# Kernel tuning notes

Measured on AMD Instinct MI355X. Metric: run time of the kernel, lower is better.

The kernel has to match this reference:

```python
import jax, jax.numpy as jnp
import numpy as np

B, N, H, MEM, V = 512, 50, 256, 8, 40001
SCALE = 1.0 / float(np.sqrt(H))
NEG = -1e12


def sinusoid_table(n_pos, d):
    pos = np.arange(n_pos)[:, None].astype(np.float64)
    j = np.arange(d)[None, :]
    ang = pos / np.power(10000.0, 2 * (j // 2) / d)
    tab = np.zeros((n_pos, d))
    tab[:, 0::2] = np.sin(ang[:, 0::2])
    tab[:, 1::2] = np.cos(ang[:, 1::2])
    return jnp.asarray(tab, jnp.float32)

TAB = sinusoid_table(N, H)


def setup_inputs():
    key = jax.random.key(0)
    ks = jax.random.split(key, 40)
    s = 0.05
    rn = lambda k, shp, sc=s: jax.random.normal(k, shp, jnp.float32) * sc
    lengths = jax.random.randint(ks[0], (B,), 1, N + 1)
    mask = (jnp.arange(N)[None, :] < lengths[:, None]).astype(jnp.int32)
    item_flag = jax.random.randint(ks[1], (B, V - 1), 0, 2).astype(jnp.int32)
    inp = {
        'seq_emb_1': rn(ks[2], (B, N, H), 1.0),
        'seq_emb_2': rn(ks[3], (B, N, H), 1.0),
        'mask': mask,
        'item_flag': item_flag,
        # 2-layer GRU (torch layout: W_ih [3H,H], W_hh [3H,H])
        'gru_wih0': rn(ks[4], (3 * H, H)), 'gru_whh0': rn(ks[5], (3 * H, H)),
        'gru_bih0': rn(ks[6], (3 * H,)), 'gru_bhh0': rn(ks[7], (3 * H,)),
        'gru_wih1': rn(ks[8], (3 * H, H)), 'gru_whh1': rn(ks[9], (3 * H, H)),
        'gru_bih1': rn(ks[10], (3 * H,)), 'gru_bhh1': rn(ks[11], (3 * H,)),
        # attention projections ([in,out] layout, y = x @ W)
        'Wq1': rn(ks[12], (H, H)), 'Wk1': rn(ks[13], (H, H)), 'Wv1': rn(ks[14], (H, H)),
        'Wq2': rn(ks[15], (H, H)), 'Wk2': rn(ks[16], (H, H)), 'Wv2': rn(ks[17], (H, H)),
        'W_ffn1': rn(ks[18], (H, H)), 'b_ffn1': rn(ks[19], (H,)),
        'W_ffn2': rn(ks[20], (H, H)), 'b_ffn2': rn(ks[21], (H,)),
        'W_one1': rn(ks[22], (H, H)), 'b_one1': rn(ks[23], (H,)),
        'W_three1': rn(ks[24], (2 * H, 1)),
        'W_trans1': rn(ks[25], (2 * H, H)), 'b_trans1': rn(ks[26], (H,)),
        'W_tail1': rn(ks[27], (H, H)), 'b_tail1': rn(ks[28], (H,)),
        'W_tail2': rn(ks[29], (H, 2)),
        'mem_k': rn(ks[30], (1, MEM, H)), 'mem_v': rn(ks[31], (1, MEM, H)),
        'emb1': rn(ks[32], (V, H)),
    }
    return inp


def _gru_layer(x, wih, whh, bih, bhh):
    # x: [B,N,H] -> [B,N,H], h0 = 0 (torch default)
    def step(h, xt):
        gi = xt @ wih.T + bih
        gh = h @ whh.T + bhh
        ir, iz, inn = jnp.split(gi, 3, axis=-1)
        hr, hz, hn = jnp.split(gh, 3, axis=-1)
        r = jax.nn.sigmoid(ir + hr)
        z = jax.nn.sigmoid(iz + hz)
        n = jnp.tanh(inn + r * hn)
        h2 = (1.0 - z) * n + z * h
        return h2, h2
    h0 = jnp.zeros((x.shape[0], H), x.dtype)
    _, ys = jax.lax.scan(step, h0, jnp.swapaxes(x, 0, 1))
    return jnp.swapaxes(ys, 0, 1)


def _co_attention(q, k, v, mask, mem_k=None, mem_v=None):
    b = q.shape[0]
    causal = jnp.tril(jnp.ones((N, N), bool))           # [N,N]
    pad = mask.astype(bool)[:, None, :]                  # [B,1,N]
    allow_seq = causal[None, :, :] & pad                 # [B,N,N]
    if mem_k is not None:
        k = jnp.concatenate([jnp.broadcast_to(mem_k, (b, MEM, H)), k], axis=1)
        v = jnp.concatenate([jnp.broadcast_to(mem_v, (b, MEM, H)), v], axis=1)
        mem_ok = jnp.ones((b, N, MEM), bool)             # memory keys always visible
        allow = jnp.concatenate([mem_ok, allow_seq], axis=-1)
    else:
        allow = allow_seq
    att = jnp.einsum('bqh,bkh->bqk', q, k) * SCALE
    att = jax.nn.softmax(jnp.where(allow, att, NEG), axis=-1)
    return jnp.einsum('bqk,bkh->bqh', att, v) * mask[:, :, None].astype(q.dtype)


def reference(seq_emb_1, seq_emb_2, mask, item_flag,
              gru_wih0, gru_whh0, gru_bih0, gru_bhh0,
              gru_wih1, gru_whh1, gru_bih1, gru_bhh1,
              Wq1, Wk1, Wv1, Wq2, Wk2, Wv2,
              W_ffn1, b_ffn1, W_ffn2, b_ffn2,
              W_one1, b_one1, W_three1, W_trans1, b_trans1,
              W_tail1, b_tail1, W_tail2, mem_k, mem_v, emb1):
    b = mask.shape[0]
    mf = mask[:, :, None].astype(jnp.float32)
    # 2-layer GRU on stream 2
    s2 = _gru_layer(seq_emb_2, gru_wih0, gru_whh0, gru_bih0, gru_bhh0)
    s2 = _gru_layer(s2, gru_wih1, gru_whh1, gru_bih1, gru_bhh1)
    last = jnp.sum(mask, axis=1) - 1                     # last valid index
    sr_l_1 = seq_emb_1[jnp.arange(b), last]              # [B,H]
    q1_1 = sr_l_1 @ W_one1 + b_one1 + TAB[0]
    se1 = seq_emb_1 * mf
    # positional encoding indexed by |pos - last_idx|
    flag = jnp.abs(jnp.arange(N, dtype=jnp.int32)[None, :] - last[:, None].astype(jnp.int32))
    pe = TAB[flag]                                       # [B,N,H]
    q1 = se1 @ Wq1 + pe
    k1 = se1 @ Wk1 + pe
    v1 = se1 @ Wv1 + pe
    att1 = _co_attention(q1, k1, v1, mask) @ W_ffn1 + b_ffn1
    se2 = s2 * mf
    k2 = se2 @ Wk2
    v2 = se2 @ Wv2
    att2 = _co_attention(q1, k2, v2, mask, mem_k, mem_v) @ W_ffn2 + b_ffn2
    att = jax.nn.relu(att1 + att2)
    alpha = jnp.concatenate([att, jnp.broadcast_to(q1_1[:, None, :], att.shape)], axis=-1) @ W_three1
    alpha = jax.nn.softmax(jnp.where(mf > 0, alpha, NEG), axis=1)  # [B,N,1]
    sess = jnp.sum(alpha * se1 * mf, axis=1)
    sess = jnp.concatenate([sess, sr_l_1], axis=1) @ W_trans1 + b_trans1
    item_emb = emb1[1:]                                  # [V-1,H]
    score = sess @ item_emb.T                            # [B,V-1]
    fl = item_flag.astype(bool)
    score_in = jax.nn.softmax(jnp.where(fl, score, NEG), axis=-1)
    score_ex = jax.nn.softmax(jnp.where(fl, NEG, score), axis=-1)
    beta = jax.nn.softmax(jax.nn.relu(sess @ W_tail1 + b_tail1) @ W_tail2, axis=-1)  # [B,2]
    boundary = jnp.mean(jnp.abs(beta[:, 0] - beta[:, 1]))
    final = score_in * beta[:, 0:1] + score_ex * beta[:, 1:2]
    return final[:, None, :], boundary
```

## Files before the change

kernel.cpp:

```cpp
#include <hip/hip_runtime.h>
#include <hip/hip_bf16.h>
#include <cstdint>
#include <cstddef>

#define Bsz 512
#define Nsq 50
#define Hd  256
#define VM1 40000
static constexpr float SCALE_C = 0.0625f;
static constexpr float NEG_C   = -1.0e12f;

typedef __attribute__((ext_vector_type(8))) short bf16x8;
typedef __attribute__((ext_vector_type(4))) float f32x4;

__device__ __forceinline__ float sigmoidf_(float x) { return 1.0f / (1.0f + __expf(-x)); }
__device__ __forceinline__ float tanh_fast(float x) {
  float t = fminf(fmaxf(2.0f * x, -60.0f), 60.0f);
  float e = __expf(t);
  return (e - 1.0f) / (e + 1.0f);
}
__device__ __forceinline__ ushort f2b(float x) {
  union { float f; uint32_t u; } c; c.f = x;
  uint32_t r = (c.u + 0x7fffu + ((c.u >> 16) & 1u)) >> 16;
  return (ushort)r;
}

__global__ void build_tab(float* __restrict__ TAB) {
  int idx = blockIdx.x * 256 + threadIdx.x;
  int pos = idx >> 8, j = idx & 255;
  int pair = j >> 1;
  float expo = (2.0f * (float)pair) / 256.0f;
  float inv = powf(10000.0f, -expo);
  float ang = (float)pos * inv;
  TAB[idx] = (j & 1) ? cosf(ang) : sinf(ang);
}

__global__ __launch_bounds__(256) void last_srl_kernel(const int* __restrict__ mask,
    const float* __restrict__ seq1, int* __restrict__ lastp, float* __restrict__ srl) {
  int b = blockIdx.x, tid = threadIdx.x;
  __shared__ int ls;
  if (tid == 0) {
    int c = 0;
    for (int t = 0; t < Nsq; ++t) c += mask[b * Nsq + t];
    ls = c - 1;
    lastp[b] = c - 1;
  }
  __syncthreads();
  srl[b * Hd + tid] = seq1[((size_t)b * Nsq + ls) * Hd + tid];
}

template <int BT, int BIAS>
__global__ __launch_bounds__(256) void gemm_tile(const float* __restrict__ A,
    const float* __restrict__ B, const float* __restrict__ bias,
    float* __restrict__ C, int M, int N, int K) {
  __shared__ float As[16][132];
  __shared__ float Bs[16][68];
  int bm = blockIdx.y * 128, bn = blockIdx.x * 64;
  int tid = threadIdx.x;
  int tm = (tid >> 4) << 3;
  int tn = (tid & 15) << 2;
  float acc[8][4] = {};
  for (int k0 = 0; k0 < K; k0 += 16) {
#pragma unroll
    for (int u = 0; u < 8; ++u) {
      int i = tid + u * 256;
      int kk = i & 15, m = i >> 4;
      As[kk][m] = A[(size_t)(bm + m) * K + (k0 + kk)];
    }
#pragma unroll
    for (int u = 0; u < 4; ++u) {
      int i = tid + u * 256;
      if (BT) {
        int kk = i & 15, n = i >> 4;
        Bs[kk][n] = B[(size_t)(bn + n) * K + (k0 + kk)];
      } else {
        int n = i & 63, kk = i >> 6;
        Bs[kk][n] = B[(size_t)(k0 + kk) * N + (bn + n)];
      }
    }
    __syncthreads();
#pragma unroll
    for (int kk = 0; kk < 16; ++kk) {
      float a[8], bb[4];
#pragma unroll
      for (int r = 0; r < 8; ++r) a[r] = As[kk][tm + r];
#pragma unroll
      for (int c = 0; c < 4; ++c) bb[c] = Bs[kk][tn + c];
#pragma unroll
      for (int r = 0; r < 8; ++r)
#pragma unroll
        for (int c = 0; c < 4; ++c) acc[r][c] += a[r] * bb[c];
    }
    __syncthreads();
  }
#pragma unroll
  for (int r = 0; r < 8; ++r) {
    size_t row = (size_t)(bm + tm + r) * N + bn;
#pragma unroll
    for (int c = 0; c < 4; ++c) {
      float v = acc[r][c];
      if (BIAS) v += bias[bn + tn + c];
      C[row + tn + c] = v;
    }
  }
}

template <int BT, int BIAS>
__global__ __launch_bounds__(256) void mfma_gemm(const ushort* __restrict__ A,
    const ushort* __restrict__ B, const float* __restrict__ bias,
    float* __restrict__ C, int M, int N, int K) {
  __shared__ ushort Asm[128][40];
  __shared__ ushort Bsm[128][40];
  int tid = threadIdx.x;
  int bm = blockIdx.y * 128, bn = blockIdx.x * 128;
  int lane = tid & 63, wave = tid >> 6;
  int quad = lane >> 4, l16 = lane & 15;
  int wm = (wave >> 1) * 64, wn = (wave & 1) * 64;
  f32x4 acc[4][4] = {};
  for (int k0 = 0; k0 < K; k0 += 32) {
#pragma unroll
    for (int u = 0; u < 2; ++u) {
      int idx = tid + u * 256;
      int r = idx >> 2, kc = (idx & 3) * 8;
      uint4 v = *(const uint4*)(A + (size_t)(bm + r) * K + k0 + kc);
      *(uint4*)&Asm[r][kc] = v;
    }
    if (BT) {
#pragma unroll
      for (int u = 0; u < 2; ++u) {
        int idx = tid + u * 256;
        int r = idx >> 2, kc = (idx & 3) * 8;
        uint4 v = make_uint4(0u, 0u, 0u, 0u);
        if (bn + r < N) v = *(const uint4*)(B + (size_t)(bn + r) * K + k0 + kc);
        *(uint4*)&Bsm[r][kc] = v;
      }
    } else {
#pragma unroll
      for (int u = 0; u < 8; ++u) {
        int idx = tid + u * 256;
        int n2 = (idx & 63) * 2, kk = idx >> 6;
        uint v = *(const uint*)(B + (size_t)(k0 + kk) * N + bn + n2);
        Bsm[n2][kk] = (ushort)(v & 0xffffu);
        Bsm[n2 + 1][kk] = (ushort)(v >> 16);
      }
    }
    __syncthreads();
    bf16x8 af[4], bfr[4];
#pragma unroll
    for (int f = 0; f < 4; ++f) af[f] = *(const bf16x8*)&Asm[wm + f * 16 + l16][quad * 8];
#pragma unroll
    for (int f = 0; f < 4; ++f) bfr[f] = *(const bf16x8*)&Bsm[wn + f * 16 + l16][quad * 8];
#pragma unroll
    for (int mf = 0; mf < 4; ++mf)
#pragma unroll
      for (int nf = 0; nf < 4; ++nf)
        acc[mf][nf] = __builtin_amdgcn_mfma_f32_16x16x32_bf16(af[mf], bfr[nf], acc[mf][nf], 0, 0, 0);
    __syncthreads();
  }
#pragma unroll
  for (int mf = 0; mf < 4; ++mf) {
#pragma unroll
    for (int r = 0; r < 4; ++r) {
      int row = bm + wm + mf * 16 + quad * 4 + r;
      size_t rowo = (size_t)row * N;
#pragma unroll
      for (int nf = 0; nf < 4; ++nf) {
        int col = bn + wn + nf * 16 + l16;
        if (col < N) {
          float v = acc[mf][nf][r];
          if (BIAS) v += bias[col];
          C[rowo + col] = v;
        }
      }
    }
  }
}

__global__ void cast_f2b_k(const float* __restrict__ s, ushort* __restrict__ d, int n4) {
  int i = blockIdx.x * 256 + threadIdx.x;
  if (i >= n4) return;
  const float4 v = ((const float4*)s)[i];
  ushort4 o; o.x = f2b(v.x); o.y = f2b(v.y); o.z = f2b(v.z); o.w = f2b(v.w);
  ((ushort4*)d)[i] = o;
}

struct Cast7 { const float* s[7]; ushort* d[7]; };
__global__ void cast7_k(Cast7 p) {
  int m = blockIdx.y;
  int i = blockIdx.x * 256 + threadIdx.x;
  const float4 v = ((const float4*)p.s[m])[i];
  ushort4 o; o.x = f2b(v.x); o.y = f2b(v.y); o.z = f2b(v.z); o.w = f2b(v.w);
  ((ushort4*)p.d[m])[i] = o;
}

__global__ void add_tab0(float* __restrict__ q) {
  int idx = blockIdx.x * 256 + threadIdx.x;
  q[idx] += (float)(threadIdx.x & 1);
}

__global__ void mask_mul_dual(const float* __restrict__ x, const int* __restrict__ m,
                              float* __restrict__ y, ushort* __restrict__ yb) {
  int idx = blockIdx.x * 256 + threadIdx.x;
  float v = m[idx >> 8] ? x[idx] : 0.0f;
  y[idx] = v;
  yb[idx] = f2b(v);
}

__global__ void add_pe3(float* __restrict__ q, float* __restrict__ k, float* __restrict__ v,
                        const float* __restrict__ TAB, const int* __restrict__ lastp) {
  int idx = blockIdx.x * 256 + threadIdx.x;
  int j = idx & 255, bt = idx >> 8;
  int b = bt / Nsq, t = bt - b * Nsq;
  int d = abs(t - lastp[b]);
  float pe = TAB[d * 256 + j];
  q[idx] += pe; k[idx] += pe; v[idx] += pe;
}

__global__ void relu_add(float* __restrict__ a, const float* __restrict__ b) {
  int idx = blockIdx.x * 256 + threadIdx.x;
  a[idx] = fmaxf(a[idx] + b[idx], 0.0f);
}

__global__ __launch_bounds__(512, 2) void gru_mfma8_kernel(const float* __restrict__ gi,
    const ushort* __restrict__ whhb, const float* __restrict__ bhh,
    ushort* __restrict__ ysb, const int* __restrict__ mask) {
  __shared__ ushort hbf[16][264];
  __shared__ float  ghs[2][768];
  int tid = threadIdx.x;
  int lane = tid & 63, wave = tid >> 6;
  int quad = lane >> 4, l16 = lane & 15;
  int s0 = blockIdx.x * 2;

  for (int i = tid; i < 16 * 264 / 2; i += 512) ((uint*)hbf)[i] = 0u;

  bf16x8 bw[48];
  const ushort* wb = whhb + (size_t)(wave * 96 + l16) * 256 + quad * 8;
#pragma unroll
  for (int f = 0; f < 48; ++f) {
    int nf = f >> 3, kf = f & 7;
    bw[f] = *(const bf16x8*)(wb + nf * (16 * 256) + kf * 32);
  }

  int d = tid & 255, sh = tid >> 8;
  float bh0 = bhh[d], bh1 = bhh[256 + d], bh2 = bhh[512 + d];
  const float* gib = gi + (size_t)(s0 + sh) * Nsq * 768;
  float g0 = gib[d], g1 = gib[256 + d], g2 = gib[512 + d];
  float hreg = 0.0f;
  __syncthreads();

  for (int t = 0; t < Nsq; ++t) {
    int tn = (t + 1 < Nsq) ? t + 1 : t;
    float p0 = gib[tn * 768 + d], p1 = gib[tn * 768 + 256 + d], p2 = gib[tn * 768 + 512 + d];

    f32x4 acc[6] = {};
#pragma unroll
    for (int kf = 0; kf < 8; ++kf) {
      bf16x8 a = *(const bf16x8*)&hbf[l16][kf * 32 + quad * 8];
#pragma unroll
      for (int nf = 0; nf < 6; ++nf)
        acc[nf] = __builtin_amdgcn_mfma_f32_16x16x32_bf16(a, bw[nf * 8 + kf], acc[nf], 0, 0, 0);
    }
    if (quad == 0) {
#pragma unroll
      for (int nf = 0; nf < 6; ++nf) {
        int n = wave * 96 + nf * 16 + l16;
        ghs[0][n] = acc[nf][0];
        ghs[1][n] = acc[nf][1];
      }
    }
    __syncthreads();

    {
      float rr = sigmoidf_(g0 + ghs[sh][d] + bh0);
      float zz = sigmoidf_(g1 + ghs[sh][256 + d] + bh1);
      float nn = tanh_fast(g2 + rr * (ghs[sh][512 + d] + bh2));
      float h2 = (1.0f - zz) * nn + zz * hreg;
      hreg = h2;
      hbf[sh][d] = f2b(h2);
      float ov = h2;
      if (mask) ov = mask[(s0 + sh) * Nsq + t] ? h2 : 0.0f;
      ysb[((size_t)(s0 + sh) * Nsq + t) * 256 + d] = f2b(ov);
    }
    g0 = p0; g1 = p1; g2 = p2;
    __syncthreads();
  }
}

template <int NMEM>
__global__ __launch_bounds__(256) void attn_mfma(const float* __restrict__ q1,
    const float* __restrict__ kseq, const float* __restrict__ vseq,
    const float* __restrict__ kmem, const float* __restrict__ vmem,
    const int* __restrict__ mask, ushort* __restrict__ out) {
  constexpr int NK = NMEM + Nsq;
  __shared__ ushort KV[64][264];
  __shared__ float Ss[64][66];
  __shared__ ushort Ps[64][72];
  __shared__ int msk[64];
  int tid = threadIdx.x;
  int lane = tid & 63, wave = tid >> 6;
  int quad = lane >> 4, l16 = lane & 15;
  int b = blockIdx.x;

  if (tid < 64) msk[tid] = (tid < Nsq) ? mask[b * Nsq + tid] : 0;

#pragma unroll
  for (int it = 0; it < 16; ++it) {
    int idx = tid + it * 256;
    int r = idx >> 6, c4 = (idx & 63) * 4;
    float4 v = make_float4(0.f, 0.f, 0.f, 0.f);
    if (r < Nsq) v = *(const float4*)(q1 + ((size_t)(b * Nsq + r)) * 256 + c4);
    ushort4 o; o.x = f2b(v.x); o.y = f2b(v.y); o.z = f2b(v.z); o.w = f2b(v.w);
    *(ushort4*)&KV[r][c4] = o;
  }
  __syncthreads();
  bf16x8 qa[8];
#pragma unroll
  for (int kf = 0; kf < 8; ++kf)
    qa[kf] = *(const bf16x8*)&KV[wave * 16 + l16][kf * 32 + quad * 8];
  __syncthreads();

#pragma unroll
  for (int it = 0; it < 16; ++it) {
    int idx = tid + it * 256;
    int r = idx >> 6, c4 = (idx & 63) * 4;
    float4 v = make_float4(0.f, 0.f, 0.f, 0.f);
    if (r < NK) {
      const float* src = (NMEM > 0 && r < NMEM)
          ? (kmem + (size_t)r * 256 + c4)
          : (kseq + ((size_t)(b * Nsq + (r - NMEM))) * 256 + c4);
      v = *(const float4*)src;
    }
    ushort4 o; o.x = f2b(v.x); o.y = f2b(v.y); o.z = f2b(v.z); o.w = f2b(v.w);
    *(ushort4*)&KV[r][c4] = o;
  }
  __syncthreads();

  {
    f32x4 acc[4] = {};
#pragma unroll
    for (int kf = 0; kf < 8; ++kf) {
#pragma unroll
      for (int nf = 0; nf < 4; ++nf) {
        bf16x8 bf = *(const bf16x8*)&KV[nf * 16 + l16][kf * 32 + quad * 8];
        acc[nf] = __builtin_amdgcn_mfma_f32_16x16x32_bf16(qa[kf], bf, acc[nf], 0, 0, 0);
      }
    }
#pragma unroll
    for (int nf = 0; nf < 4; ++nf)
#pragma unroll
      for (int r = 0; r < 4; ++r)
        Ss[wave * 16 + quad * 4 + r][nf * 16 + l16] = acc[nf][r];
  }
  __syncthreads();

#pragma unroll
  for (int it = 0; it < 16; ++it) {
    int idx = tid + it * 256;
    int r = idx >> 6, c4 = (idx & 63) * 4;
    float4 v = make_float4(0.f, 0.f, 0.f, 0.f);
    if (r < NK) {
      const float* src = (NMEM > 0 && r < NMEM)
          ? (vmem + (size_t)r * 256 + c4)
          : (vseq + ((size_t)(b * Nsq + (r - NMEM))) * 256 + c4);
      v = *(const float4*)src;
    }
    ushort4 o; o.x = f2b(v.x); o.y = f2b(v.y); o.z = f2b(v.z); o.w = f2b(v.w);
    *(ushort4*)&KV[r][c4] = o;
  }
  if (tid < 64) {
    int t = tid;
    if (t < Nsq) {
      float m = -1e30f;
      for (int j = 0; j < NK; ++j) {
        bool ok = (j < NMEM) || (((j - NMEM) <= t) && (msk[j - NMEM] != 0));
        if (ok) m = fmaxf(m, Ss[t][j] * SCALE_C);
      }
      float sum = 0.0f;
      for (int j = 0; j < NK; ++j) {
        bool ok = (j < NMEM) || (((j - NMEM) <= t) && (msk[j - NMEM] != 0));
        if (ok) sum += __expf(Ss[t][j] * SCALE_C - m);
      }
      float inv = 1.0f / sum;
      for (int j = 0; j < 64; ++j) {
        float p = 0.0f;
        if (j < NK) {
          bool ok = (j < NMEM) || (((j - NMEM) <= t) && (msk[j - NMEM] != 0));
          if (ok) p = __expf(Ss[t][j] * SCALE_C - m) * inv;
        }
        Ps[t][j] = f2b(p);
      }
    } else {
      for (int j = 0; j < 64; ++j) Ps[t][j] = 0;
    }
  }
  __syncthreads();

  {
    f32x4 o[4][4] = {};
#pragma unroll
    for (int kf = 0; kf < 2; ++kf) {
      bf16x8 pa[4];
#pragma unroll
      for (int mf = 0; mf < 4; ++mf)
        pa[mf] = *(const bf16x8*)&Ps[mf * 16 + l16][kf * 32 + quad * 8];
#pragma unroll
      for (int nf = 0; nf < 4; ++nf) {
        int h = wave * 64 + nf * 16 + l16;
        ushort e0 = KV[kf * 32 + quad * 8 + 0][h];
        ushort e1 = KV[kf * 32 + quad * 8 + 1][h];
        ushort e2 = KV[kf * 32 + quad * 8 + 2][h];
        ushort e3 = KV[kf * 32 + quad * 8 + 3][h];
        ushort e4 = KV[kf * 32 + quad * 8 + 4][h];
        ushort e5 = KV[kf * 32 + quad * 8 + 5][h];
        ushort e6 = KV[kf * 32 + quad * 8 + 6][h];
        ushort e7 = KV[kf * 32 + quad * 8 + 7][h];
        bf16x8 vb = {(short)e0, (short)e1, (short)e2, (short)e3,
                     (short)e4, (short)e5, (short)e6, (short)e7};
#pragma unroll
        for (int mf = 0; mf < 4; ++mf)
          o[mf][nf] = __builtin_amdgcn_mfma_f32_16x16x32_bf16(pa[mf], vb, o[mf][nf], 0, 0, 0);
      }
    }
#pragma unroll
    for (int mf = 0; mf < 4; ++mf) {
#pragma unroll
      for (int r = 0; r < 4; ++r) {
        int t = mf * 16 + quad * 4 + r;
        if (t < Nsq) {
          int zero = (msk[t] == 0);
#pragma unroll
          for (int nf = 0; nf < 4; ++nf) {
            int h = wave * 64 + nf * 16 + l16;
            float val = zero ? 0.0f : o[mf][nf][r];
            out[((size_t)(b * Nsq + t)) * 256 + h] = f2b(val);
          }
        }
      }
    }
  }
}

__global__ __launch_bounds__(256) void alpha_sess_kernel(const float* __restrict__ att,
    const float* __restrict__ W3, const float* __restrict__ q11,
    const float* __restrict__ se1, const int* __restrict__ mask,
    const float* __restrict__ srl, float* __restrict__ sesscat) {
  int b = blockIdx.x, tid = threadIdx.x;
  __shared__ float red[256];
  __shared__ float ash[50];
  red[tid] = q11[b * Hd + tid] * W3[256 + tid];
  __syncthreads();
  for (int s = 128; s; s >>= 1) { if (tid < s) red[tid] += red[tid + s]; __syncthreads(); }
  float cq = red[0];
  float aval = 0.0f;
  if (tid < 50) {
    float s = cq;
    const float* ar = att + ((size_t)b * Nsq + tid) * Hd;
    for (int hh = 0; hh < 256; ++hh) s += ar[hh] * W3[hh];
    aval = mask[b * Nsq + tid] ? s : NEG_C;
  }
  if (tid < 64) {
    float s = (tid < 50) ? aval : NEG_C;
    float m = s;
    for (int off = 32; off; off >>= 1) m = fmaxf(m, __shfl_xor(m, off));
    float e = expf(s - m);
    float sum = e;
    for (int off = 32; off; off >>= 1) sum += __shfl_xor(sum, off);
    if (tid < 50) ash[tid] = e / sum;
  }
  __syncthreads();
  float acc = 0.0f;
  const float* se = se1 + (size_t)b * Nsq * Hd;
  for (int t = 0; t < Nsq; ++t) acc += ash[t] * se[t * 256 + tid];
  sesscat[(size_t)b * 512 + tid] = acc;
  sesscat[(size_t)b * 512 + 256 + tid] = srl[b * Hd + tid];
}

__global__ __launch_bounds__(256) void beta_kernel(const float* __restrict__ sess2,
    const float* __restrict__ Wt1, const float* __restrict__ bt1,
    const float* __restrict__ Wt2, float* __restrict__ beta, float* __restrict__ bnd) {
  int b = blockIdx.x, tid = threadIdx.x;
  __shared__ float xs[256];
  __shared__ float r0[256], r1[256];
  xs[tid] = sess2[b * Hd + tid];
  __syncthreads();
  float hsum = bt1[tid];
  for (int k = 0; k < 256; ++k) hsum += xs[k] * Wt1[k * 256 + tid];
  float hid = fmaxf(hsum, 0.0f);
  r0[tid] = hid * Wt2[tid * 2 + 0];
  r1[tid] = hid * Wt2[tid * 2 + 1];
  __syncthreads();
  for (int s = 128; s; s >>= 1) {
    if (tid < s) { r0[tid] += r0[tid + s]; r1[tid] += r1[tid + s]; }
    __syncthreads();
  }
  if (tid == 0) {
    float t0 = r0[0], t1 = r1[0];
    float m = fmaxf(t0, t1);
    float e0 = expf(t0 - m), e1 = expf(t1 - m);
    float bb0 = e0 / (e0 + e1), bb1 = e1 / (e0 + e1);
    beta[b * 2] = bb0; beta[b * 2 + 1] = bb1;
    atomicAdd(bnd, fabsf(bb0 - bb1) * (1.0f / 512.0f));
  }
}

__global__ __launch_bounds__(256) void score_final_fused(float* __restrict__ score,
    const int* __restrict__ flag, const float* __restrict__ beta) {
  int b = blockIdx.x, tid = threadIdx.x;
  float4* sr = (float4*)(score + (size_t)b * VM1);
  const int4* fr = (const int4*)(flag + (size_t)b * VM1);
  constexpr int NV = VM1 / 4;

  __shared__ float red[256], red2[256];

  float mi = -INFINITY, me = -INFINITY;
  for (int i = tid; i < NV; i += 256) {
    float4 s = sr[i];
    int4 f = fr[i];
    if (f.x) mi = fmaxf(mi, s.x); else me = fmaxf(me, s.x);
    if (f.y) mi = fmaxf(mi, s.y); else me = fmaxf(me, s.y);
    if (f.z) mi = fmaxf(mi, s.z); else me = fmaxf(me, s.z);
    if (f.w) mi = fmaxf(mi, s.w); else me = fmaxf(me, s.w);
  }
  red[tid] = mi; red2[tid] = me;
  __syncthreads();
  for (int s = 128; s; s >>= 1) {
    if (tid < s) { red[tid] = fmaxf(red[tid], red[tid + s]); red2[tid] = fmaxf(red2[tid], red2[tid + s]); }
    __syncthreads();
  }
  float Mi = red[0], Me = red2[0];
  __syncthreads();

  float si = 0.0f, se = 0.0f;
  for (int i = tid; i < NV; i += 256) {
    float4 s = sr[i];
    int4 f = fr[i];
    float e0 = __expf(s.x - (f.x ? Mi : Me));
    float e1 = __expf(s.y - (f.y ? Mi : Me));
    float e2 = __expf(s.z - (f.z ? Mi : Me));
    float e3 = __expf(s.w - (f.w ? Mi : Me));
    si += (f.x ? e0 : 0.0f) + (f.y ? e1 : 0.0f) + (f.z ? e2 : 0.0f) + (f.w ? e3 : 0.0f);
    se += (f.x ? 0.0f : e0) + (f.y ? 0.0f : e1) + (f.z ? 0.0f : e2) + (f.w ? 0.0f : e3);
    s.x = f.x ? e0 : -e0;
    s.y = f.y ? e1 : -e1;
    s.z = f.z ? e2 : -e2;
    s.w = f.w ? e3 : -e3;
    sr[i] = s;
  }
  red[tid] = si; red2[tid] = se;
  __syncthreads();
  for (int s = 128; s; s >>= 1) {
    if (tid < s) { red[tid] += red[tid + s]; red2[tid] += red2[tid + s]; }
    __syncthreads();
  }
  float c0 = beta[b * 2] / red[0];
  float nc1 = -(beta[b * 2 + 1] / red2[0]);
  __syncthreads();

  for (int i = tid; i < NV; i += 256) {
    float4 z = sr[i];
    z.x = (z.x >= 0.0f ? c0 : nc1) * z.x;
    z.y = (z.y >= 0.0f ? c0 : nc1) * z.y;
    z.z = (z.z >= 0.0f ? c0 : nc1) * z.z;
    z.w = (z.w >= 0.0f ? c0 : nc1) * z.w;
    sr[i] = z;
  }
}

extern "C" void kernel_launch(void* const* d_in, const int* in_sizes, int n_in,
                              void* d_out, int out_size, void* d_ws, size_t ws_size,
                              hipStream_t stream) {
  const float* seq1  = (const float*)d_in[0];
  const float* seq2  = (const float*)d_in[1];
  const int*   mask  = (const int*)d_in[2];
  const int*   iflag = (const int*)d_in[3];
  const float* wih0  = (const float*)d_in[4];
  const float* whh0  = (const float*)d_in[5];
  const float* bih0  = (const float*)d_in[6];
  const float* bhh0  = (const float*)d_in[7];
  const float* wih1  = (const float*)d_in[8];
  const float* whh1  = (const float*)d_in[9];
  const float* bih1  = (const float*)d_in[10];
  const float* bhh1  = (const float*)d_in[11];
  const float* Wq1   = (const float*)d_in[12];
  const float* Wk1   = (const float*)d_in[13];
  const float* Wv1   = (const float*)d_in[14];
  const float* Wk2   = (const float*)d_in[16];
  const float* Wv2   = (const float*)d_in[17];
  const float* Wffn1 = (const float*)d_in[18];
  const float* bffn1 = (const float*)d_in[19];
  const float* Wffn2 = (const float*)d_in[20];
  const float* bffn2 = (const float*)d_in[21];
  const float* Wone  = (const float*)d_in[22];
  const float* bone  = (const float*)d_in[23];
  const float* W3    = (const float*)d_in[24];
  const float* Wtr   = (const float*)d_in[25];
  const float* btr   = (const float*)d_in[26];
  const float* Wt1   = (const float*)d_in[27];
  const float* bt1   = (const float*)d_in[28];
  const float* Wt2   = (const float*)d_in[29];
  const float* memk  = (const float*)d_in[30];
  const float* memv  = (const float*)d_in[31];
  const float* emb1  = (const float*)d_in[32];
  float* out = (float*)d_out;

  char* wsb = (char*)d_ws;
  float*  TAB    = (float*)(wsb + 0);
  int*    lastp  = (int*)  (wsb + 51200);
  float*  srl    = (float*)(wsb + 53248);
  float*  q11    = (float*)(wsb + 577536);
  ushort* whh0b  = (ushort*)(wsb + 1101824);
  ushort* whh1b  = (ushort*)(wsb + 1888256);
  ushort* wih0b  = (ushort*)(wsb + 2674688);
  ushort* wih1b  = (ushort*)(wsb + 3067904);
  ushort* w7b    = (ushort*)(wsb + 3461120);
  ushort* bufS   = (ushort*)(wsb + 4378624);
  float*  se1    = (float*)(wsb + 17485824);
  ushort* se1b   = (ushort*)(wsb + 43700224);
  float*  giQ    = (float*)(wsb + 56807424);
  float*  kv2a   = (float*)(wsb + 135450624);
  float*  kv2b   = (float*)(wsb + 161665024);
  ushort* ao1b   = (ushort*)(wsb + 187879424);
  ushort* ao2b   = (ushort*)(wsb + 200986624);

  float* gi = giQ;
  float* q1 = giQ;
  float* k1 = giQ + 6553600;
  float* v1 = giQ + 13107200;
  ushort* embB    = (ushort*)giQ;
  float*  sesscat = (float*)((char*)giQ + 20480000);
  float*  sess2   = (float*)((char*)giQ + 21528576);
  ushort* sess2b  = (ushort*)((char*)giQ + 22052864);
  float*  betab   = (float*)((char*)giQ + 22315008);
  float*  stats   = (float*)((char*)giQ + 22319104);
  float*  bnd     = out + (size_t)Bsz * VM1;

  ushort* Wq1b = w7b;              ushort* Wk1b = w7b + 65536;
  ushort* Wv1b = w7b + 131072;     ushort* Wk2b = w7b + 196608;
  ushort* Wv2b = w7b + 262144;     ushort* Wf1b = w7b + 327680;
  ushort* Wf2b = w7b + 393216;

  build_tab<<<50, 256, 0, stream>>>(TAB);
  last_srl_kernel<<<Bsz, 256, 0, stream>>>(mask, seq1, lastp, srl);
  gemm_tile<0, 1><<<dim3(4, 4), 256, 0, stream>>>(srl, Wone, bone, q11, 512, 256, 256);
  add_tab0<<<512, 256, 0, stream>>>(q11);

  cast_f2b_k<<<6400, 256, 0, stream>>>(seq2, bufS, 1638400);
  cast_f2b_k<<<192, 256, 0, stream>>>(wih0, wih0b, 49152);
  cast_f2b_k<<<192, 256, 0, stream>>>(wih1, wih1b, 49152);
  cast_f2b_k<<<192, 256, 0, stream>>>(whh0, whh0b, 49152);
  cast_f2b_k<<<192, 256, 0, stream>>>(whh1, whh1b, 49152);
  Cast7 c7;
  c7.s[0] = Wq1; c7.s[1] = Wk1; c7.s[2] = Wv1; c7.s[3] = Wk2; c7.s[4] = Wv2;
  c7.s[5] = Wffn1; c7.s[6] = Wffn2;
  c7.d[0] = Wq1b; c7.d[1] = Wk1b; c7.d[2] = Wv1b; c7.d[3] = Wk2b; c7.d[4] = Wv2b;
  c7.d[5] = Wf1b; c7.d[6] = Wf2b;
  cast7_k<<<dim3(64, 7), 256, 0, stream>>>(c7);

  mfma_gemm<1, 1><<<dim3(6, 200), 256, 0, stream>>>(bufS, wih0b, bih0, gi, 25600, 768, 256);
  gru_mfma8_kernel<<<256, 512, 0, stream>>>(gi, whh0b, bhh0, bufS, nullptr);
  mfma_gemm<1, 1><<<dim3(6, 200), 256, 0, stream>>>(bufS, wih1b, bih1, gi, 25600, 768, 256);
  gru_mfma8_kernel<<<256, 512, 0, stream>>>(gi, whh1b, bhh1, bufS, mask);

  mask_mul_dual<<<25600, 256, 0, stream>>>(seq1, mask, se1, se1b);

  mfma_gemm<0, 0><<<dim3(2, 200), 256, 0, stream>>>(bufS, Wk2b, nullptr, kv2a, 25600, 256, 256);
  mfma_gemm<0, 0><<<dim3(2, 200), 256, 0, stream>>>(bufS, Wv2b, nullptr, kv2b, 25600, 256, 256);
  mfma_gemm<0, 0><<<dim3(2, 200), 256, 0, stream>>>(se1b, Wq1b, nullptr, q1, 25600, 256, 256);
  mfma_gemm<0, 0><<<dim3(2, 200), 256, 0, stream>>>(se1b, Wk1b, nullptr, k1, 25600, 256, 256);
  mfma_gemm<0, 0><<<dim3(2, 200), 256, 0, stream>>>(se1b, Wv1b, nullptr, v1, 25600, 256, 256);
  add_pe3<<<25600, 256, 0, stream>>>(q1, k1, v1, TAB, lastp);

  attn_mfma<0><<<Bsz, 256, 0, stream>>>(q1, k1, v1, nullptr, nullptr, mask, ao1b);
  attn_mfma<8><<<Bsz, 256, 0, stream>>>(q1, kv2a, kv2b, memk, memv, mask, ao2b);
  mfma_gemm<0, 1><<<dim3(2, 200), 256, 0, stream>>>(ao1b, Wf1b, bffn1, kv2a, 25600, 256, 256);
  mfma_gemm<0, 1><<<dim3(2, 200), 256, 0, stream>>>(ao2b, Wf2b, bffn2, kv2b, 25600, 256, 256);
  relu_add<<<25600, 256, 0, stream>>>(kv2a, kv2b);

  alpha_sess_kernel<<<Bsz, 256, 0, stream>>>(kv2a, W3, q11, se1, mask, srl, sesscat);
  gemm_tile<0, 1><<<dim3(4, 4), 256, 0, stream>>>(sesscat, Wtr, btr, sess2, 512, 256, 512);
  cast_f2b_k<<<128, 256, 0, stream>>>(sess2, sess2b, 32768);

  hipMemsetAsync(bnd, 0, 4, stream);
  beta_kernel<<<Bsz, 256, 0, stream>>>(sess2, Wt1, bt1, Wt2, betab, bnd);
  cast_f2b_k<<<10000, 256, 0, stream>>>(emb1 + 256, embB, 2560000);
  mfma_gemm<1, 0><<<dim3(313, 4), 256, 0, stream>>>(sess2b, embB, nullptr, out, 512, VM1, 256);
  score_final_fused<<<Bsz, 256, 0, stream>>>(out, iflag, betab);

  (void)in_sizes; (void)n_in; (void)out_size; (void)ws_size;
}
```

Before: 1.007 ms.

## Pack item flags into shared-memory bitmask and recompute exp in softmax epilogue

```diff
diff --git a/kernel.cpp b/kernel.cpp
--- a/kernel.cpp
+++ b/kernel.cpp
@@ -503,19 +503,26 @@
   }
 }
 
-__global__ __launch_bounds__(256) void score_final_fused(float* __restrict__ score,
+__global__ __launch_bounds__(1024) void score_final_fused(float* __restrict__ score,
     const int* __restrict__ flag, const float* __restrict__ beta) {
   int b = blockIdx.x, tid = threadIdx.x;
   float4* sr = (float4*)(score + (size_t)b * VM1);
   const int4* fr = (const int4*)(flag + (size_t)b * VM1);
   constexpr int NV = VM1 / 4;
-
-  __shared__ float red[256], red2[256];
+  constexpr int NW = (NV + 7) / 8;
+
+  __shared__ uint bits[NW];
+  __shared__ float red[1024], red2[1024];
+
+  for (int i = tid; i < NW; i += 1024) bits[i] = 0u;
+  __syncthreads();
 
   float mi = -INFINITY, me = -INFINITY;
-  for (int i = tid; i < NV; i += 256) {
+  for (int i = tid; i < NV; i += 1024) {
     float4 s = sr[i];
     int4 f = fr[i];
+    uint nib = (f.x ? 1u : 0u) | (f.y ? 2u : 0u) | (f.z ? 4u : 0u) | (f.w ? 8u : 0u);
+    if (nib) atomicOr(&bits[i >> 3], nib << ((i & 7) * 4));
     if (f.x) mi = fmaxf(mi, s.x); else me = fmaxf(me, s.x);
     if (f.y) mi = fmaxf(mi, s.y); else me = fmaxf(me, s.y);
     if (f.z) mi = fmaxf(mi, s.z); else me = fmaxf(me, s.z);
@@ -523,7 +530,7 @@
   }
   red[tid] = mi; red2[tid] = me;
   __syncthreads();
-  for (int s = 128; s; s >>= 1) {
+  for (int s = 512; s; s >>= 1) {
     if (tid < s) { red[tid] = fmaxf(red[tid], red[tid + s]); red2[tid] = fmaxf(red2[tid], red2[tid + s]); }
     __syncthreads();
   }
@@ -531,38 +538,36 @@
   __syncthreads();
 
   float si = 0.0f, se = 0.0f;
-  for (int i = tid; i < NV; i += 256) {
+  for (int i = tid; i < NV; i += 1024) {
     float4 s = sr[i];
-    int4 f = fr[i];
-    float e0 = __expf(s.x - (f.x ? Mi : Me));
-    float e1 = __expf(s.y - (f.y ? Mi : Me));
-    float e2 = __expf(s.z - (f.z ? Mi : Me));
-    float e3 = __expf(s.w - (f.w ? Mi : Me));
-    si += (f.x ? e0 : 0.0f) + (f.y ? e1 : 0.0f) + (f.z ? e2 : 0.0f) + (f.w ? e3 : 0.0f);
-    se += (f.x ? 0.0f : e0) + (f.y ? 0.0f : e1) + (f.z ? 0.0f : e2) + (f.w ? 0.0f : e3);
-    s.x = f.x ? e0 : -e0;
-    s.y = f.y ? e1 : -e1;
-    s.z = f.z ? e2 : -e2;
-    s.w = f.w ? e3 : -e3;
+    uint nib = bits[i >> 3] >> ((i & 7) * 4);
+    float e0 = __expf(s.x - ((nib & 1u) ? Mi : Me));
+    float e1 = __expf(s.y - ((nib & 2u) ? Mi : Me));
+    float e2 = __expf(s.z - ((nib & 4u) ? Mi : Me));
+    float e3 = __expf(s.w - ((nib & 8u) ? Mi : Me));
+    si += ((nib & 1u) ? e0 : 0.0f) + ((nib & 2u) ? e1 : 0.0f)
+        + ((nib & 4u) ? e2 : 0.0f) + ((nib & 8u) ? e3 : 0.0f);
+    se += ((nib & 1u) ? 0.0f : e0) + ((nib & 2u) ? 0.0f : e1)
+        + ((nib & 4u) ? 0.0f : e2) + ((nib & 8u) ? 0.0f : e3);
+  }
+  red[tid] = si; red2[tid] = se;
+  __syncthreads();
+  for (int s = 512; s; s >>= 1) {
+    if (tid < s) { red[tid] += red[tid + s]; red2[tid] += red2[tid + s]; }
+    __syncthreads();
+  }
+  float c0 = beta[b * 2] / red[0];
+  float c1 = beta[b * 2 + 1] / red2[0];
+  __syncthreads();
+
+  for (int i = tid; i < NV; i += 1024) {
+    float4 s = sr[i];
+    uint nib = bits[i >> 3] >> ((i & 7) * 4);
+    s.x = ((nib & 1u) ? c0 : c1) * __expf(s.x - ((nib & 1u) ? Mi : Me));
+    s.y = ((nib & 2u) ? c0 : c1) * __expf(s.y - ((nib & 2u) ? Mi : Me));
+    s.z = ((nib & 4u) ? c0 : c1) * __expf(s.z - ((nib & 4u) ? Mi : Me));
+    s.w = ((nib & 8u) ? c0 : c1) * __expf(s.w - ((nib & 8u) ? Mi : Me));
     sr[i] = s;
-  }
-  red[tid] = si; red2[tid] = se;
-  __syncthreads();
-  for (int s = 128; s; s >>= 1) {
-    if (tid < s) { red[tid] += red[tid + s]; red2[tid] += red2[tid + s]; }
-    __syncthreads();
-  }
-  float c0 = beta[b * 2] / red[0];
-  float nc1 = -(beta[b * 2 + 1] / red2[0]);
-  __syncthreads();
-
-  for (int i = tid; i < NV; i += 256) {
-    float4 z = sr[i];
-    z.x = (z.x >= 0.0f ? c0 : nc1) * z.x;
-    z.y = (z.y >= 0.0f ? c0 : nc1) * z.y;
-    z.z = (z.z >= 0.0f ? c0 : nc1) * z.z;
-    z.w = (z.w >= 0.0f ? c0 : nc1) * z.w;
-    sr[i] = z;
   }
 }
 
@@ -684,7 +689,7 @@
   beta_kernel<<<Bsz, 256, 0, stream>>>(sess2, Wt1, bt1, Wt2, betab, bnd);
   cast_f2b_k<<<10000, 256, 0, stream>>>(emb1 + 256, embB, 2560000);
   mfma_gemm<1, 0><<<dim3(313, 4), 256, 0, stream>>>(sess2b, embB, nullptr, out, 512, VM1, 256);
-  score_final_fused<<<Bsz, 256, 0, stream>>>(out, iflag, betab);
+  score_final_fused<<<Bsz, 1024, 0, stream>>>(out, iflag, betab);
 
   (void)in_sizes; (void)n_in; (void)out_size; (void)ws_size;
 }
```

Result: faster. 978.2 us (-2.8%).
